# Optimization experiments

Hardware: AMD Instinct MI355X
Metric: run time of the kernel (lower is better)

Reference implementation:

```python
import jax, jax.numpy as jnp
import numpy as np

IMG = 84
CH = 64
OUT = 5
PARAM_KEYS = ['w0', 'b0', 'w1', 'b1', 'w2', 'b2', 'w3', 'b3', 'fc_w', 'fc_b']


def _conv(x, w, b):
    # x: [C,H,W], w: [O,I,3,3] -> [O,H,W] (SAME padding, stride 1)
    y = jax.lax.conv_general_dilated(x[None], w, (1, 1), 'SAME',
                                     dimension_numbers=('NCHW', 'OIHW', 'NCHW'))[0]
    return y + b[:, None, None]


def _pool(x):
    # 2x2 max pool, VALID (84->42->21->10->5)
    return jax.lax.reduce_window(x, -jnp.inf, jax.lax.max, (1, 2, 2), (1, 2, 2), 'VALID')


def _fnet_single(params, x):
    # x: flat [3*84*84] -> logits [OUT]; mirrors fnet_single(params, x) on unsqueezed input
    h = x.reshape(3, IMG, IMG)
    for i in range(4):
        h = _pool(jax.nn.relu(_conv(h, params['w%d' % i], params['b%d' % i])))
    h = h.reshape(-1)  # [CH*5*5]
    return params['fc_w'] @ h + params['fc_b']


def setup_inputs() -> dict:
    key = jax.random.key(0)
    ks = jax.random.split(key, 16)
    N = 64
    x1 = jax.random.normal(ks[0], (N, 3 * IMG * IMG), jnp.float32)
    x2 = jax.random.normal(ks[1], (N, 3 * IMG * IMG), jnp.float32)
    params = {}
    cin = 3
    for i in range(4):
        fan_in = cin * 9
        params['w%d' % i] = jax.random.normal(ks[2 + i], (CH, cin, 3, 3), jnp.float32) * (2.0 / fan_in) ** 0.5
        params['b%d' % i] = jnp.zeros((CH,), jnp.float32)
        cin = CH
    feat = CH * 5 * 5
    params['fc_w'] = jax.random.normal(ks[6], (OUT, feat), jnp.float32) * (1.0 / feat) ** 0.5
    params['fc_b'] = jnp.zeros((OUT,), jnp.float32)
    scalings = jax.random.uniform(ks[7], (len(PARAM_KEYS),), jnp.float32, 0.5, 1.5)
    inp = {'x1': x1, 'x2': x2, 'scalings': scalings, 'c': 2}
    inp.update(params)
    return inp


def reference(x1, x2, w0, b0, w1, b1, w2, b2, w3, b3, fc_w, fc_b, scalings, c):
    params = {'w0': w0, 'b0': b0, 'w1': w1, 'b1': b1, 'w2': w2, 'b2': b2,
              'w3': w3, 'b3': b3, 'fc_w': fc_w, 'fc_b': fc_b}
    jac_fn = jax.vmap(jax.jacrev(_fnet_single), in_axes=(None, 0))
    jac1 = jac_fn(params, x1)  # dict: [N, OUT, *param_shape]
    jac2 = jac_fn(params, x2)  # dict: [M, OUT, *param_shape]
    N, M = x1.shape[0], x2.shape[0]
    K = jnp.zeros((N, M, OUT), x1.dtype)
    for idx, k in enumerate(PARAM_KEYS):  # fixed small loop over parameter tensors
        j1 = (scalings[idx] * jac1[k]).reshape(N, OUT, -1)
        j2 = (scalings[idx] * jac2[k]).reshape(M, OUT, -1)
        K = K + jnp.einsum('Naf,Maf->NMa', j1, j2)
    return K[:, :, c]  # [N, M]
```

## Files before the change

kernel.cpp:

```cpp
#include <hip/hip_runtime.h>
#include <cstdint>

constexpr int OFF_W1 = 0;
constexpr int OFF_B1 = 1728;
constexpr int OFF_W2 = 1792;
constexpr int OFF_B2 = 38656;
constexpr int OFF_W3 = 38720;
constexpr int OFF_B3 = 75584;
constexpr int OFF_W4 = 75648;
constexpr int OFF_B4 = 112512;
constexpr int OFF_H  = 112576;
constexpr int PJ     = 114176;

__global__ __launch_bounds__(256) void k_transpose(
    const float* __restrict__ x1, const float* __restrict__ x2, float* __restrict__ xT)
{
    __shared__ float tile[32][33];
    const int c0 = blockIdx.x * 32, s0 = blockIdx.y * 32;
    const int tx = threadIdx.x, ty = threadIdx.y;
#pragma unroll
    for (int k = 0; k < 4; ++k) {
        const int row = s0 + ty + k * 8;
        const int col = c0 + tx;
        const float* src = (row < 64) ? (x1 + (size_t)row * 21168)
                                      : (x2 + (size_t)(row - 64) * 21168);
        tile[ty + k * 8][tx] = (col < 21168) ? src[col] : 0.f;
    }
    __syncthreads();
#pragma unroll
    for (int k = 0; k < 4; ++k) {
        const int c = c0 + ty + k * 8;
        if (c < 21168) xT[(size_t)c * 128 + (s0 + tx)] = tile[tx][ty + k * 8];
    }
}

__global__ __launch_bounds__(256) void k_wprep(
    const float* __restrict__ w1, const float* __restrict__ w2,
    const float* __restrict__ w3, const float* __restrict__ w4,
    float* __restrict__ wS1, float* __restrict__ wS2, float* __restrict__ wS3,
    float* __restrict__ wS4, float* __restrict__ wB2, float* __restrict__ wB3,
    float* __restrict__ wB4)
{
    const int idx = blockIdx.x * 256 + threadIdx.x;
    if (idx >= 36864) return;
    const int o = idx / 576, rem = idx % 576, i = rem / 9, t = rem % 9;
    wS2[(i * 9 + t) * 64 + o] = w2[idx];
    wS3[(i * 9 + t) * 64 + o] = w3[idx];
    wS4[(i * 9 + t) * 64 + o] = w4[idx];
    wB2[(o * 9 + (8 - t)) * 64 + i] = w2[idx];
    wB3[(o * 9 + (8 - t)) * 64 + i] = w3[idx];
    wB4[(o * 9 + (8 - t)) * 64 + i] = w4[idx];
    if (idx < 1728) {
        const int o1 = idx / 27, r1 = idx % 27, i1 = r1 / 9, t1 = r1 % 9;
        wS1[(i1 * 9 + t1) * 64 + o1] = w1[idx];
    }
}

template<int CIN, int TIN, int OB, int SI, int SY, int SX>
__global__ __launch_bounds__(256) void k_fwd(
    const float* __restrict__ in, const float* __restrict__ wS,
    const float* __restrict__ bias, float* __restrict__ pout,
    unsigned char* __restrict__ mout)
{
    constexpr int PW = TIN / 2;
    const int lane = threadIdx.x;
    const int x0 = blockIdx.x * 4;
    const int o0 = blockIdx.y * OB;
    const int pr = blockIdx.z * 2 + threadIdx.y;
    if (pr >= PW) return;
    const int cr0 = 2 * pr;

    float acc[OB][2][4];
#pragma unroll
    for (int j = 0; j < OB; ++j)
#pragma unroll
        for (int r = 0; r < 2; ++r)
#pragma unroll
            for (int p = 0; p < 4; ++p) acc[j][r][p] = 0.f;

#pragma unroll 1
    for (int i = 0; i < CIN; ++i) {
        float a[4][6];
#pragma unroll
        for (int rr = 0; rr < 4; ++rr) {
            const int y = cr0 - 1 + rr;
            const bool rok = (unsigned)y < (unsigned)TIN;
#pragma unroll
            for (int cc = 0; cc < 6; ++cc) {
                const int x = x0 - 1 + cc;
                a[rr][cc] = (rok && (unsigned)x < (unsigned)TIN)
                    ? in[(size_t)i * SI + (size_t)y * SY + (size_t)x * SX + lane] : 0.f;
            }
        }
        const float* wrow = wS + (i * 9) * 64 + o0;
#pragma unroll
        for (int t = 0; t < 9; ++t) {
            const int dy = t / 3, dx = t % 3;
#pragma unroll
            for (int j = 0; j < OB; ++j) {
                const float wv = wrow[t * 64 + j];
#pragma unroll
                for (int r = 0; r < 2; ++r)
#pragma unroll
                    for (int p = 0; p < 4; ++p)
                        acc[j][r][p] = fmaf(wv, a[r + dy][p + dx], acc[j][r][p]);
            }
        }
    }
#pragma unroll
    for (int j = 0; j < OB; ++j) {
        const float b = bias[o0 + j];
#pragma unroll
        for (int q = 0; q < 2; ++q) {
            const int wx = x0 / 2 + q;
            if (wx >= PW) continue;
            const float c00 = fmaxf(acc[j][0][2 * q]     + b, 0.f);
            const float c01 = fmaxf(acc[j][0][2 * q + 1] + b, 0.f);
            const float c10 = fmaxf(acc[j][1][2 * q]     + b, 0.f);
            const float c11 = fmaxf(acc[j][1][2 * q + 1] + b, 0.f);
            float best = c00; int idx = 0;
            if (c01 > best) { best = c01; idx = 1; }
            if (c10 > best) { best = c10; idx = 2; }
            if (c11 > best) { best = c11; idx = 3; }
            const size_t oi = ((size_t)(pr * PW + wx) * 64 + (o0 + j)) * 128 + lane;
            pout[oi] = best;
            mout[oi] = (unsigned char)(idx | (best > 0.f ? 4 : 0));
        }
    }
}

__global__ __launch_bounds__(128) void k_seed(
    const float* __restrict__ fcw, const int* __restrict__ cptr,
    const float* __restrict__ p4, const float* __restrict__ scal_,
    float* __restrict__ g4, float* __restrict__ JT)
{
    const int s = threadIdx.x;
    const int cell = blockIdx.x / 64, o = blockIdx.x % 64;
    const int c = *cptr;
    const int j = o * 25 + cell;
    const size_t base = ((size_t)cell * 64 + o) * 128 + s;
    g4[base] = fcw[(size_t)c * 1600 + j];
    JT[(size_t)(OFF_H + j) * 128 + s] = scal_[8] * p4[base];
}

template<int TL, int TP, int OB>
__global__ __launch_bounds__(256) void k_bwd(
    const float* __restrict__ gl, const unsigned char* __restrict__ ml,
    const float* __restrict__ wB, float* __restrict__ gout)
{
    const int lane = threadIdx.x;
    const int x0 = blockIdx.x * 4;
    const int i0 = blockIdx.y * OB;
    const int row = blockIdx.z * 2 + threadIdx.y;
    if (row >= TP) return;

    float acc[OB][4];
#pragma unroll
    for (int j = 0; j < OB; ++j)
#pragma unroll
        for (int p = 0; p < 4; ++p) acc[j][p] = 0.f;

#pragma unroll 1
    for (int o = 0; o < 64; ++o) {
        float a[3][6];
#pragma unroll
        for (int rr = 0; rr < 3; ++rr) {
            const int y = row - 1 + rr;
            const bool rok = (unsigned)y < (unsigned)TP;
            const int wy = y >> 1;
            const int yb = (y & 1) << 1;
#pragma unroll
            for (int cc = 0; cc < 6; ++cc) {
                const int x = x0 - 1 + cc;
                float v = 0.f;
                if (rok && (unsigned)x < (unsigned)TP) {
                    const int wx = x >> 1;
                    if (wy < TL && wx < TL) {
                        const size_t base = ((size_t)(wy * TL + wx) * 64 + o) * 128 + lane;
                        const int code = 4 | yb | (x & 1);
                        const int mv = ml[base];
                        const float gv = gl[base];
                        v = (mv == code) ? gv : 0.f;
                    }
                }
                a[rr][cc] = v;
            }
        }
        const float* wrow = wB + (o * 9) * 64 + i0;
#pragma unroll
        for (int t = 0; t < 9; ++t) {
            const int dy = t / 3, dx = t % 3;
#pragma unroll
            for (int j = 0; j < OB; ++j) {
                const float wv = wrow[t * 64 + j];
#pragma unroll
                for (int p = 0; p < 4; ++p)
                    acc[j][p] = fmaf(wv, a[dy][p + dx], acc[j][p]);
            }
        }
    }
#pragma unroll
    for (int j = 0; j < OB; ++j)
#pragma unroll
        for (int p = 0; p < 4; ++p) {
            const int x = x0 + p;
            if (x < TP)
                gout[((size_t)(row * TP + x) * 64 + (i0 + j)) * 128 + lane] = acc[j][p];
        }
}

template<int TL, int TIN, bool SPLIT>
__global__ __launch_bounds__(128) void k_wgrad(
    const float* __restrict__ gl, const unsigned char* __restrict__ ml,
    const float* __restrict__ h, const float* __restrict__ scal_,
    const int scalIdx, const int joff, float* __restrict__ JT, const int ychunk)
{
    const int s = threadIdx.x;
    const int o0 = blockIdx.x * 2, i0 = blockIdx.y * 2;
    const int y0 = blockIdx.z * ychunk;
    const int y1 = (y0 + ychunk < TIN) ? y0 + ychunk : TIN;

    float acc[2][2][9];
#pragma unroll
    for (int a = 0; a < 2; ++a)
#pragma unroll
        for (int b = 0; b < 2; ++b)
#pragma unroll
            for (int t = 0; t < 9; ++t) acc[a][b][t] = 0.f;

#pragma unroll 1
    for (int y = y0; y < y1; ++y) {
        const int wy = y >> 1;
        const int ybit = (y & 1) << 1;
        float hw[2][3][3];
#pragma unroll
        for (int ji = 0; ji < 2; ++ji)
#pragma unroll
            for (int dy = 0; dy < 3; ++dy) {
                const int ry = y + dy - 1;
                const bool rok = (unsigned)ry < (unsigned)TIN;
                hw[ji][dy][2] = 0.f;
                hw[ji][dy][1] = 0.f;
                hw[ji][dy][0] = rok ? h[((size_t)(ry * TIN) * 64 + i0 + ji) * 128 + s] : 0.f;
            }
#pragma unroll 1
        for (int xb = 0; xb < ((TIN + 2) / 3) * 3; xb += 3) {
#pragma unroll
            for (int k = 0; k < 3; ++k) {
                const int x = xb + k;
                const int xn = x + 1;
                const bool cok = xn < TIN;
#pragma unroll
                for (int ji = 0; ji < 2; ++ji)
#pragma unroll
                    for (int dy = 0; dy < 3; ++dy) {
                        const int ry = y + dy - 1;
                        hw[ji][dy][(k + 1) % 3] =
                            (cok && (unsigned)ry < (unsigned)TIN)
                                ? h[((size_t)(ry * TIN + xn) * 64 + i0 + ji) * 128 + s] : 0.f;
                    }
                if (x < TIN) {
                    const int wx = x >> 1;
                    const bool uok = (wy < TL) && (wx < TL);
                    const int code = 4 | ybit | (x & 1);
                    float u[2] = {0.f, 0.f};
                    if (uok) {
#pragma unroll
                        for (int jo = 0; jo < 2; ++jo) {
                            const size_t base = ((size_t)(wy * TL + wx) * 64 + o0 + jo) * 128 + s;
                            const int mv = ml[base];
                            const float gv = gl[base];
                            u[jo] = (mv == code) ? gv : 0.f;
                        }
                    }
#pragma unroll
                    for (int jo = 0; jo < 2; ++jo)
#pragma unroll
                        for (int ji = 0; ji < 2; ++ji)
#pragma unroll
                            for (int dy = 0; dy < 3; ++dy)
#pragma unroll
                                for (int dx = 0; dx < 3; ++dx)
                                    acc[jo][ji][dy * 3 + dx] =
                                        fmaf(u[jo], hw[ji][dy][(k + dx + 2) % 3],
                                             acc[jo][ji][dy * 3 + dx]);
                }
            }
        }
    }
    const float sc = scal_[scalIdx];
#pragma unroll
    for (int jo = 0; jo < 2; ++jo)
#pragma unroll
        for (int ji = 0; ji < 2; ++ji)
#pragma unroll
            for (int t = 0; t < 9; ++t) {
                const int feat = joff + ((o0 + jo) * 64 + (i0 + ji)) * 9 + t;
                const float v = sc * acc[jo][ji][t];
                if (SPLIT) atomicAdd(&JT[(size_t)feat * 128 + s], v);
                else JT[(size_t)feat * 128 + s] = v;
            }
}

__global__ __launch_bounds__(128) void k_wgrad1(
    const float* __restrict__ g1, const unsigned char* __restrict__ m1,
    const float* __restrict__ xT, const float* __restrict__ scal_,
    float* __restrict__ JT)
{
    const int s = threadIdx.x;
    const int o0 = blockIdx.x * 2;
    const int wy = blockIdx.y;

    float acc[2][3][9];
#pragma unroll
    for (int oo = 0; oo < 2; ++oo)
#pragma unroll
        for (int i = 0; i < 3; ++i)
#pragma unroll
            for (int t = 0; t < 9; ++t) acc[oo][i][t] = 0.f;

    float hw[3][4][3];
#pragma unroll
    for (int i = 0; i < 3; ++i)
#pragma unroll
        for (int r = 0; r < 4; ++r) {
            const int ry = 2 * wy - 1 + r;
            hw[i][r][2] = 0.f;
            hw[i][r][1] = 0.f;
            hw[i][r][0] = ((unsigned)ry < 84u)
                ? xT[((size_t)i * 7056 + ry * 84) * 128 + s] : 0.f;
        }
    const int cellrow = wy * 42;

#pragma unroll 1
    for (int xb = 0; xb < 84; xb += 3) {
#pragma unroll
        for (int k = 0; k < 3; ++k) {
            const int x = xb + k;
            const int xn = x + 1;
            const bool cok = xn < 84;
#pragma unroll
            for (int i = 0; i < 3; ++i)
#pragma unroll
                for (int r = 0; r < 4; ++r) {
                    const int ry = 2 * wy - 1 + r;
                    hw[i][r][(k + 1) % 3] = (cok && (unsigned)ry < 84u)
                        ? xT[((size_t)i * 7056 + ry * 84 + xn) * 128 + s] : 0.f;
                }
            const int wx = x >> 1;
            const int xbit = x & 1;
            float u[2][2];
#pragma unroll
            for (int oo = 0; oo < 2; ++oo) {
                const size_t base = ((size_t)(cellrow + wx) * 64 + o0 + oo) * 128 + s;
                const int mv = m1[base];
                const float gv = g1[base];
                u[oo][0] = (mv == (4 | 0 | xbit)) ? gv : 0.f;
                u[oo][1] = (mv == (4 | 2 | xbit)) ? gv : 0.f;
            }
#pragma unroll
            for (int oo = 0; oo < 2; ++oo)
#pragma unroll
                for (int yy = 0; yy < 2; ++yy)
#pragma unroll
                    for (int i = 0; i < 3; ++i)
#pragma unroll
                        for (int dy = 0; dy < 3; ++dy)
#pragma unroll
                            for (int dx = 0; dx < 3; ++dx)
                                acc[oo][i][dy * 3 + dx] =
                                    fmaf(u[oo][yy], hw[i][yy + dy][(k + dx + 2) % 3],
                                         acc[oo][i][dy * 3 + dx]);
        }
    }
    const float sc = scal_[0];
#pragma unroll
    for (int oo = 0; oo < 2; ++oo)
#pragma unroll
        for (int i = 0; i < 3; ++i)
#pragma unroll
            for (int t = 0; t < 9; ++t)
                atomicAdd(&JT[(size_t)(OFF_W1 + (o0 + oo) * 27 + i * 9 + t) * 128 + s],
                          sc * acc[oo][i][t]);
}

__global__ __launch_bounds__(128) void k_dbpart(
    const float* __restrict__ g1, const float* __restrict__ g2,
    const float* __restrict__ g3, const float* __restrict__ g4,
    const unsigned char* __restrict__ m1, const unsigned char* __restrict__ m2,
    const unsigned char* __restrict__ m3, const unsigned char* __restrict__ m4,
    float* __restrict__ part)
{
    const int s = threadIdx.x;
    const int o = blockIdx.x, chunk = blockIdx.y, layer = blockIdx.z;
    const float* g; const unsigned char* m; int nc;
    if (layer == 0)      { g = g1; m = m1; nc = 1764; }
    else if (layer == 1) { g = g2; m = m2; nc = 441; }
    else if (layer == 2) { g = g3; m = m3; nc = 100; }
    else                 { g = g4; m = m4; nc = 25; }
    const int c0 = chunk * nc / 4, c1 = (chunk + 1) * nc / 4;
    float acc = 0.f;
    for (int cell = c0; cell < c1; ++cell) {
        const size_t base = ((size_t)cell * 64 + o) * 128 + s;
        acc += (m[base] & 4) ? g[base] : 0.f;
    }
    part[((size_t)(layer * 4 + chunk) * 64 + o) * 128 + s] = acc;
}

__global__ __launch_bounds__(256) void k_dbred(
    const float* __restrict__ part, const float* __restrict__ scal_,
    float* __restrict__ JT)
{
    const int idx = blockIdx.x * 256 + threadIdx.x;
    const int layer = idx >> 13, o = (idx >> 7) & 63, s = idx & 127;
    float v = 0.f;
#pragma unroll
    for (int ch = 0; ch < 4; ++ch)
        v += part[((size_t)(layer * 4 + ch) * 64 + o) * 128 + s];
    const int offb[4] = {OFF_B1, OFF_B2, OFF_B3, OFF_B4};
    JT[(size_t)(offb[layer] + o) * 128 + s] = scal_[2 * layer + 1] * v;
}

__global__ __launch_bounds__(256) void k_ntk(const float* __restrict__ JT,
                                             float* __restrict__ part)
{
    __shared__ float As[32][64], Bs[32][64];
    const int tx = threadIdx.x, ty = threadIdx.y;
    const int t = ty * 16 + tx;
    float acc[4][4];
#pragma unroll
    for (int a = 0; a < 4; ++a)
#pragma unroll
        for (int b = 0; b < 4; ++b) acc[a][b] = 0.f;

    for (int ch = 0; ch < 16; ++ch) {
        const int k0 = (blockIdx.x * 16 + ch) * 32;
        __syncthreads();
#pragma unroll
        for (int q = 0; q < 4; ++q) {
            const int fidx = q * 256 + t;
            const int row = fidx >> 5;
            const int c4 = (fidx & 31) * 4;
            const float4 v = *(const float4*)&JT[(size_t)(k0 + row) * 128 + c4];
            if (c4 < 64) *(float4*)&As[row][c4] = v;
            else         *(float4*)&Bs[row][c4 - 64] = v;
        }
        __syncthreads();
#pragma unroll
        for (int k = 0; k < 32; ++k) {
            const float4 av = *(const float4*)&As[k][ty * 4];
            const float4 bv = *(const float4*)&Bs[k][tx * 4];
            acc[0][0] = fmaf(av.x, bv.x, acc[0][0]);
            acc[0][1] = fmaf(av.x, bv.y, acc[0][1]);
            acc[0][2] = fmaf(av.x, bv.z, acc[0][2]);
            acc[0][3] = fmaf(av.x, bv.w, acc[0][3]);
            acc[1][0] = fmaf(av.y, bv.x, acc[1][0]);
            acc[1][1] = fmaf(av.y, bv.y, acc[1][1]);
            acc[1][2] = fmaf(av.y, bv.z, acc[1][2]);
            acc[1][3] = fmaf(av.y, bv.w, acc[1][3]);
            acc[2][0] = fmaf(av.z, bv.x, acc[2][0]);
            acc[2][1] = fmaf(av.z, bv.y, acc[2][1]);
            acc[2][2] = fmaf(av.z, bv.z, acc[2][2]);
            acc[2][3] = fmaf(av.z, bv.w, acc[2][3]);
            acc[3][0] = fmaf(av.w, bv.x, acc[3][0]);
            acc[3][1] = fmaf(av.w, bv.y, acc[3][1]);
            acc[3][2] = fmaf(av.w, bv.z, acc[3][2]);
            acc[3][3] = fmaf(av.w, bv.w, acc[3][3]);
        }
    }
#pragma unroll
    for (int a = 0; a < 4; ++a)
#pragma unroll
        for (int b = 0; b < 4; ++b)
            part[(size_t)blockIdx.x * 4096 + (ty * 4 + a) * 64 + (tx * 4 + b)] = acc[a][b];
}

__global__ __launch_bounds__(256) void k_ntkred(
    const float* __restrict__ part, const float* __restrict__ scal_,
    float* __restrict__ out)
{
    const int t = blockIdx.x * 256 + threadIdx.x;
    float v = scal_[9] * scal_[9];
    for (int ck = 0; ck < 223; ++ck) v += part[(size_t)ck * 4096 + t];
    out[t] = v;
}

extern "C" void kernel_launch(void* const* d_in, const int* in_sizes, int n_in,
                              void* d_out, int out_size, void* d_ws, size_t ws_size,
                              hipStream_t stream)
{
    const void* IN[14];
    if (n_in >= 14 && in_sizes[2] == 10 && in_sizes[3] == 1) {
        for (int k = 0; k < 14; ++k) IN[k] = d_in[k];
    } else {
        IN[0] = d_in[0]; IN[1] = d_in[1];
        IN[2] = d_in[12]; IN[3] = d_in[13];
        for (int k = 0; k < 8; ++k) IN[4 + k] = d_in[2 + k];
        IN[12] = d_in[10]; IN[13] = d_in[11];
    }
    const float* x1   = (const float*)IN[0];
    const float* x2   = (const float*)IN[1];
    const float* scal = (const float*)IN[2];
    const int*   cp   = (const int*)IN[3];
    const float* w1 = (const float*)IN[4];  const float* b1 = (const float*)IN[5];
    const float* w2 = (const float*)IN[6];  const float* b2 = (const float*)IN[7];
    const float* w3 = (const float*)IN[8];  const float* b3 = (const float*)IN[9];
    const float* w4 = (const float*)IN[10]; const float* b4 = (const float*)IN[11];
    const float* fcw = (const float*)IN[12];
    float* out = (float*)d_out;

    char* base = (char*)d_ws;
    size_t off = 0;
    auto alloc = [&](size_t bytes) -> char* {
        char* p = base + off;
        off = (off + bytes + 255) & ~(size_t)255;
        return p;
    };
    float* JT = (float*)alloc((size_t)PJ * 128 * 4);
    float* xT = JT + (size_t)OFF_W3 * 128;
    float* p1 = (float*)alloc((size_t)1764 * 64 * 128 * 4);
    float* p2 = (float*)alloc((size_t)441  * 64 * 128 * 4);
    float* p3 = (float*)alloc((size_t)100  * 64 * 128 * 4);
    float* p4 = (float*)alloc((size_t)25   * 64 * 128 * 4);
    unsigned char* m1 = (unsigned char*)alloc((size_t)1764 * 64 * 128);
    unsigned char* m2 = (unsigned char*)alloc((size_t)441  * 64 * 128);
    unsigned char* m3 = (unsigned char*)alloc((size_t)100  * 64 * 128);
    unsigned char* m4 = (unsigned char*)alloc((size_t)25   * 64 * 128);
    float* g1 = (float*)alloc((size_t)1764 * 64 * 128 * 4);
    float* g2 = (float*)alloc((size_t)441  * 64 * 128 * 4);
    float* g3 = (float*)alloc((size_t)100  * 64 * 128 * 4);
    float* g4 = (float*)alloc((size_t)25   * 64 * 128 * 4);
    float* wS1 = (float*)alloc(1728 * 4);
    float* wS2 = (float*)alloc(36864 * 4);
    float* wS3 = (float*)alloc(36864 * 4);
    float* wS4 = (float*)alloc(36864 * 4);
    float* wB2 = (float*)alloc(36864 * 4);
    float* wB3 = (float*)alloc(36864 * 4);
    float* wB4 = (float*)alloc(36864 * 4);
    float* dbp = (float*)alloc((size_t)16 * 64 * 128 * 4);
    float* ntkp = g1;
    (void)ws_size;

    hipMemsetAsync(JT, 0, (size_t)OFF_B2 * 128 * 4, stream);

    k_transpose<<<dim3(662, 4), dim3(32, 8), 0, stream>>>(x1, x2, xT);
    k_wprep<<<144, 256, 0, stream>>>(w1, w2, w3, w4, wS1, wS2, wS3, wS4, wB2, wB3, wB4);

    k_fwd<3, 84, 8, 84 * 84 * 128, 84 * 128, 128>
        <<<dim3(21, 8, 21), dim3(128, 2), 0, stream>>>(xT, wS1, b1, p1, m1);
    k_fwd<64, 42, 8, 128, 42 * 64 * 128, 64 * 128>
        <<<dim3(11, 8, 11), dim3(128, 2), 0, stream>>>(p1, wS2, b2, p2, m2);
    k_fwd<64, 21, 4, 128, 21 * 64 * 128, 64 * 128>
        <<<dim3(5, 16, 5), dim3(128, 2), 0, stream>>>(p2, wS3, b3, p3, m3);
    k_fwd<64, 10, 4, 128, 10 * 64 * 128, 64 * 128>
        <<<dim3(3, 16, 3), dim3(128, 2), 0, stream>>>(p3, wS4, b4, p4, m4);

    k_seed<<<1600, 128, 0, stream>>>(fcw, cp, p4, scal, g4, JT);

    k_bwd<5, 10, 8><<<dim3(3, 8, 5),  dim3(128, 2), 0, stream>>>(g4, m4, wB4, g3);
    k_bwd<10, 21, 8><<<dim3(6, 8, 11), dim3(128, 2), 0, stream>>>(g3, m3, wB3, g2);
    k_bwd<21, 42, 8><<<dim3(11, 8, 21), dim3(128, 2), 0, stream>>>(g2, m2, wB2, g1);

    k_wgrad<5, 10, false><<<dim3(32, 32, 1), 128, 0, stream>>>(g4, m4, p3, scal, 6, OFF_W4, JT, 10);
    k_wgrad1<<<dim3(32, 42), 128, 0, stream>>>(g1, m1, xT, scal, JT);
    k_wgrad<21, 42, true><<<dim3(32, 32, 2), 128, 0, stream>>>(g2, m2, p1, scal, 2, OFF_W2, JT, 21);
    k_wgrad<10, 21, false><<<dim3(32, 32, 1), 128, 0, stream>>>(g3, m3, p2, scal, 4, OFF_W3, JT, 21);

    k_dbpart<<<dim3(64, 4, 4), 128, 0, stream>>>(g1, g2, g3, g4, m1, m2, m3, m4, dbp);
    k_dbred<<<128, 256, 0, stream>>>(dbp, scal, JT);

    k_ntk<<<223, dim3(16, 16), 0, stream>>>(JT, ntkp);
    k_ntkred<<<16, 256, 0, stream>>>(ntkp, scal, out);
}
```

Measured before the change: 2.546 ms.

## Restructure weight-gradient kernel over pooled windows with wider input-channel tile

The weight-gradient kernel now iterates over pooled output positions (wy, wx) instead of full-resolution pixels. Each loaded gradient/mask value is expanded into the four pool sub-positions, and a 4x4 input window is reused across them. Each block covers 4 input channels instead of 2, with a sliding-window register buffer, and all layers split along wy with atomic accumulation into pre-zeroed JT. This cuts redundant mask/gradient loads and skips work on non-argmax pixels, but raises register pressure and adds memsets and atomics. The NTK GEMM is also split across twice as many blocks with shorter K chunks, and the final reduction is lengthened to match.

```diff
diff --git a/kernel.cpp b/kernel.cpp
--- a/kernel.cpp
+++ b/kernel.cpp
@@ -209,81 +209,95 @@
         }
 }
 
-template<int TL, int TIN, bool SPLIT>
+template<int TL, int TIN>
 __global__ __launch_bounds__(128) void k_wgrad(
     const float* __restrict__ gl, const unsigned char* __restrict__ ml,
     const float* __restrict__ h, const float* __restrict__ scal_,
-    const int scalIdx, const int joff, float* __restrict__ JT, const int ychunk)
+    const int scalIdx, const int joff, float* __restrict__ JT, const int wychunk)
 {
     const int s = threadIdx.x;
-    const int o0 = blockIdx.x * 2, i0 = blockIdx.y * 2;
-    const int y0 = blockIdx.z * ychunk;
-    const int y1 = (y0 + ychunk < TIN) ? y0 + ychunk : TIN;
-
-    float acc[2][2][9];
-#pragma unroll
-    for (int a = 0; a < 2; ++a)
-#pragma unroll
-        for (int b = 0; b < 2; ++b)
-#pragma unroll
-            for (int t = 0; t < 9; ++t) acc[a][b][t] = 0.f;
+    const int o0 = blockIdx.x * 2;
+    const int i0 = blockIdx.y * 4;
+    const int wy0 = blockIdx.z * wychunk;
+    const int wy1 = (wy0 + wychunk < TL) ? wy0 + wychunk : TL;
+
+    float acc[2][4][9];
+#pragma unroll
+    for (int jo = 0; jo < 2; ++jo)
+#pragma unroll
+        for (int ji = 0; ji < 4; ++ji)
+#pragma unroll
+            for (int t = 0; t < 9; ++t) acc[jo][ji][t] = 0.f;
 
 #pragma unroll 1
-    for (int y = y0; y < y1; ++y) {
-        const int wy = y >> 1;
-        const int ybit = (y & 1) << 1;
-        float hw[2][3][3];
-#pragma unroll
-        for (int ji = 0; ji < 2; ++ji)
-#pragma unroll
-            for (int dy = 0; dy < 3; ++dy) {
-                const int ry = y + dy - 1;
+    for (int wy = wy0; wy < wy1; ++wy) {
+        float hw[4][4][4];
+#pragma unroll
+        for (int ji = 0; ji < 4; ++ji)
+#pragma unroll
+            for (int r = 0; r < 4; ++r) {
+                const int ry = 2 * wy - 1 + r;
                 const bool rok = (unsigned)ry < (unsigned)TIN;
-                hw[ji][dy][2] = 0.f;
-                hw[ji][dy][1] = 0.f;
-                hw[ji][dy][0] = rok ? h[((size_t)(ry * TIN) * 64 + i0 + ji) * 128 + s] : 0.f;
+                hw[ji][r][0] = 0.f;
+#pragma unroll
+                for (int c = 1; c < 4; ++c) {
+                    const int col = c - 1;
+                    hw[ji][r][c] = rok
+                        ? h[((size_t)(ry * TIN + col) * 64 + i0 + ji) * 128 + s] : 0.f;
+                }
             }
 #pragma unroll 1
-        for (int xb = 0; xb < ((TIN + 2) / 3) * 3; xb += 3) {
-#pragma unroll
-            for (int k = 0; k < 3; ++k) {
-                const int x = xb + k;
-                const int xn = x + 1;
-                const bool cok = xn < TIN;
-#pragma unroll
-                for (int ji = 0; ji < 2; ++ji)
-#pragma unroll
-                    for (int dy = 0; dy < 3; ++dy) {
-                        const int ry = y + dy - 1;
-                        hw[ji][dy][(k + 1) % 3] =
-                            (cok && (unsigned)ry < (unsigned)TIN)
-                                ? h[((size_t)(ry * TIN + xn) * 64 + i0 + ji) * 128 + s] : 0.f;
-                    }
-                if (x < TIN) {
-                    const int wx = x >> 1;
-                    const bool uok = (wy < TL) && (wx < TL);
-                    const int code = 4 | ybit | (x & 1);
-                    float u[2] = {0.f, 0.f};
-                    if (uok) {
-#pragma unroll
-                        for (int jo = 0; jo < 2; ++jo) {
-                            const size_t base = ((size_t)(wy * TL + wx) * 64 + o0 + jo) * 128 + s;
-                            const int mv = ml[base];
-                            const float gv = gl[base];
-                            u[jo] = (mv == code) ? gv : 0.f;
-                        }
-                    }
-#pragma unroll
-                    for (int jo = 0; jo < 2; ++jo)
-#pragma unroll
-                        for (int ji = 0; ji < 2; ++ji)
+        for (int wx = 0; wx < TL; ++wx) {
+            float uu[2][2][2];
+#pragma unroll
+            for (int jo = 0; jo < 2; ++jo) {
+                const size_t base = ((size_t)(wy * TL + wx) * 64 + o0 + jo) * 128 + s;
+                const int mv = ml[base];
+                const float gv = gl[base];
+#pragma unroll
+                for (int yy = 0; yy < 2; ++yy)
+#pragma unroll
+                    for (int xx = 0; xx < 2; ++xx)
+                        uu[jo][yy][xx] = (mv == (4 | (yy << 1) | xx)) ? gv : 0.f;
+            }
+#pragma unroll
+            for (int jo = 0; jo < 2; ++jo)
+#pragma unroll
+                for (int yy = 0; yy < 2; ++yy)
+#pragma unroll
+                    for (int xx = 0; xx < 2; ++xx) {
+                        const float uv = uu[jo][yy][xx];
+#pragma unroll
+                        for (int ji = 0; ji < 4; ++ji)
 #pragma unroll
                             for (int dy = 0; dy < 3; ++dy)
 #pragma unroll
                                 for (int dx = 0; dx < 3; ++dx)
                                     acc[jo][ji][dy * 3 + dx] =
-                                        fmaf(u[jo], hw[ji][dy][(k + dx + 2) % 3],
+                                        fmaf(uv, hw[ji][yy + dy][xx + dx],
                                              acc[jo][ji][dy * 3 + dx]);
+                    }
+            if (wx + 1 < TL) {
+#pragma unroll
+                for (int ji = 0; ji < 4; ++ji)
+#pragma unroll
+                    for (int r = 0; r < 4; ++r) {
+                        hw[ji][r][0] = hw[ji][r][2];
+                        hw[ji][r][1] = hw[ji][r][3];
+                    }
+#pragma unroll
+                for (int c = 2; c < 4; ++c) {
+                    const int col = 2 * wx + 1 + c;
+                    const bool cok = col < TIN;
+#pragma unroll
+                    for (int ji = 0; ji < 4; ++ji)
+#pragma unroll
+                        for (int r = 0; r < 4; ++r) {
+                            const int ry = 2 * wy - 1 + r;
+                            hw[ji][r][c] = (cok && (unsigned)ry < (unsigned)TIN)
+                                ? h[((size_t)(ry * TIN + col) * 64 + i0 + ji) * 128 + s]
+                                : 0.f;
+                        }
                 }
             }
         }
@@ -292,13 +306,11 @@
 #pragma unroll
     for (int jo = 0; jo < 2; ++jo)
 #pragma unroll
-        for (int ji = 0; ji < 2; ++ji)
+        for (int ji = 0; ji < 4; ++ji)
 #pragma unroll
             for (int t = 0; t < 9; ++t) {
                 const int feat = joff + ((o0 + jo) * 64 + (i0 + ji)) * 9 + t;
-                const float v = sc * acc[jo][ji][t];
-                if (SPLIT) atomicAdd(&JT[(size_t)feat * 128 + s], v);
-                else JT[(size_t)feat * 128 + s] = v;
+                atomicAdd(&JT[(size_t)feat * 128 + s], sc * acc[jo][ji][t]);
             }
 }
 
@@ -421,6 +433,7 @@
     JT[(size_t)(offb[layer] + o) * 128 + s] = scal_[2 * layer + 1] * v;
 }
 
+constexpr int NTK_BLOCKS = 446;
 __global__ __launch_bounds__(256) void k_ntk(const float* __restrict__ JT,
                                              float* __restrict__ part)
 {
@@ -433,8 +446,8 @@
 #pragma unroll
         for (int b = 0; b < 4; ++b) acc[a][b] = 0.f;
 
-    for (int ch = 0; ch < 16; ++ch) {
-        const int k0 = (blockIdx.x * 16 + ch) * 32;
+    for (int ch = 0; ch < 8; ++ch) {
+        const int k0 = (blockIdx.x * 8 + ch) * 32;
         __syncthreads();
 #pragma unroll
         for (int q = 0; q < 4; ++q) {
@@ -481,7 +494,7 @@
 {
     const int t = blockIdx.x * 256 + threadIdx.x;
     float v = scal_[9] * scal_[9];
-    for (int ck = 0; ck < 223; ++ck) v += part[(size_t)ck * 4096 + t];
+    for (int ck = 0; ck < NTK_BLOCKS; ++ck) v += part[(size_t)ck * 4096 + t];
     out[t] = v;
 }
 
@@ -542,6 +555,7 @@
     (void)ws_size;
 
     hipMemsetAsync(JT, 0, (size_t)OFF_B2 * 128 * 4, stream);
+    hipMemsetAsync(JT + (size_t)OFF_W4 * 128, 0, (size_t)36864 * 128 * 4, stream);
 
     k_transpose<<<dim3(662, 4), dim3(32, 8), 0, stream>>>(x1, x2, xT);
     k_wprep<<<144, 256, 0, stream>>>(w1, w2, w3, w4, wS1, wS2, wS3, wS4, wB2, wB3, wB4);
@@ -561,14 +575,15 @@
     k_bwd<10, 21, 8><<<dim3(6, 8, 11), dim3(128, 2), 0, stream>>>(g3, m3, wB3, g2);
     k_bwd<21, 42, 8><<<dim3(11, 8, 21), dim3(128, 2), 0, stream>>>(g2, m2, wB2, g1);
 
-    k_wgrad<5, 10, false><<<dim3(32, 32, 1), 128, 0, stream>>>(g4, m4, p3, scal, 6, OFF_W4, JT, 10);
+    k_wgrad<5, 10><<<dim3(32, 16, 2), 128, 0, stream>>>(g4, m4, p3, scal, 6, OFF_W4, JT, 3);
     k_wgrad1<<<dim3(32, 42), 128, 0, stream>>>(g1, m1, xT, scal, JT);
-    k_wgrad<21, 42, true><<<dim3(32, 32, 2), 128, 0, stream>>>(g2, m2, p1, scal, 2, OFF_W2, JT, 21);
-    k_wgrad<10, 21, false><<<dim3(32, 32, 1), 128, 0, stream>>>(g3, m3, p2, scal, 4, OFF_W3, JT, 21);
+    hipMemsetAsync(JT + (size_t)OFF_W3 * 128, 0, (size_t)36864 * 128 * 4, stream);
+    k_wgrad<10, 21><<<dim3(32, 16, 2), 128, 0, stream>>>(g3, m3, p2, scal, 4, OFF_W3, JT, 5);
+    k_wgrad<21, 42><<<dim3(32, 16, 3), 128, 0, stream>>>(g2, m2, p1, scal, 2, OFF_W2, JT, 7);
 
     k_dbpart<<<dim3(64, 4, 4), 128, 0, stream>>>(g1, g2, g3, g4, m1, m2, m3, m4, dbp);
     k_dbred<<<128, 256, 0, stream>>>(dbp, scal, JT);
 
-    k_ntk<<<223, dim3(16, 16), 0, stream>>>(JT, ntkp);
+    k_ntk<<<NTK_BLOCKS, dim3(16, 16), 0, stream>>>(JT, ntkp);
     k_ntkred<<<16, 256, 0, stream>>>(ntkp, scal, out);
 }
```

Result: slower. 2.924 ms (+14.9%).
